# Performance work log

Measured on AMD Instinct MI355X. Metric: run time of the kernel, lower is better.

## Reference

```python
import jax, jax.numpy as jnp
import numpy as np

# WAGE-style quantizer (NeuroSim training path): round to 2^(b-1) levels, clip to (-1+1/S, 1-1/S),
# straight-through estimator for gradients.

def wage_q(x, bits=8):
    S = 2.0 ** (bits - 1)
    q = jnp.clip(jnp.round(x * S) / S, -1.0 + 1.0 / S, 1.0 - 1.0 / S)
    return x + jax.lax.stop_gradient(q - x)


def qconv(x, w, stride, pad, wl_w=8, wl_a=8):
    wq = wage_q(w, wl_w)
    y = jax.lax.conv_general_dilated(
        x, wq, window_strides=(stride, stride),
        padding=[(pad, pad), (pad, pad)],
        dimension_numbers=('NCHW', 'OIHW', 'NCHW'))
    return wage_q(y, wl_a)


def pad_hw(x, p):
    return jnp.pad(x, ((0, 0), (0, 0), (p, p), (p, p)))


def crop_like(x, tgt):
    return x[:, :, :tgt.shape[2], :tgt.shape[3]]


WEIGHT_SHAPES = {
    'w1': (64, 4, 3, 3), 'w2': (128, 64, 3, 3), 'w3': (256, 128, 3, 3), 'w4': (512, 256, 3, 3),
    'wr11': (512, 512, 3, 3), 'wr12': (512, 512, 3, 3), 'wr21': (512, 512, 3, 3), 'wr22': (512, 512, 3, 3),
    'wd3': (128, 512, 4, 4), 'wd2': (64, 416, 4, 4), 'wd1': (4, 224, 4, 4),
    'wu43': (32, 512, 4, 4), 'wu32': (32, 416, 4, 4), 'wu21': (32, 224, 4, 4), 'wu10': (32, 100, 4, 4),
    'wfc': (1, 32),
}


def setup_inputs() -> dict:
    key = jax.random.key(0)
    keys = jax.random.split(key, len(WEIGHT_SHAPES) + 1)
    inp = {'x': jax.random.normal(keys[0], (8, 4, 256, 256), dtype=jnp.float32)}
    for i, (name, shp) in enumerate(WEIGHT_SHAPES.items()):
        fan_in = int(np.prod(shp[1:]))
        inp[name] = jax.random.normal(keys[i + 1], shp, dtype=jnp.float32) / np.sqrt(fan_in)
    return inp


def reference(x, w1, w2, w3, w4, wr11, wr12, wr21, wr22,
              wd3, wd2, wd1, wu43, wu32, wu21, wu10, wfc):
    c1 = qconv(x, w1, 2, 1)        # [B,64,128,128]
    c2 = qconv(c1, w2, 2, 1)       # [B,128,64,64]
    c3 = qconv(c2, w3, 2, 1)       # [B,256,32,32]
    c4 = qconv(c3, w4, 2, 1)       # [B,512,16,16]
    r11 = qconv(c4, wr11, 1, 1)
    r12 = (1.0 - qconv(r11, wr12, 1, 1)) * c4
    r21 = qconv(r12, wr21, 1, 1)
    r22 = (1.0 - qconv(r21, wr22, 1, 1)) * r12
    r22p = pad_hw(r22, 8)                                   # [B,512,32,32]
    flow4_up = crop_like(qconv(r22p, wu43, 1, 2), c3)       # [B,32,32,32]
    d3 = crop_like(qconv(r22p, wd3, 1, 2), c3)              # [B,128,32,32]
    cat3 = pad_hw(jnp.concatenate([c3, d3, flow4_up], 1), 16)  # [B,416,64,64]
    flow3_up = crop_like(qconv(cat3, wu32, 1, 2), c2)
    d2 = crop_like(qconv(cat3, wd2, 1, 2), c2)
    cat2 = pad_hw(jnp.concatenate([c2, d2, flow3_up], 1), 32)  # [B,224,128,128]
    flow2_up = crop_like(qconv(cat2, wu21, 1, 2), c1)
    d1 = crop_like(qconv(cat2, wd1, 1, 2), c1)
    cat1 = pad_hw(jnp.concatenate([c1, d1, flow2_up], 1), 64)  # [B,100,256,256]
    u10 = qconv(cat1, wu10, 1, 2)                              # [B,32,257,257]
    feat = jnp.max(u10, axis=(2, 3))                           # AdaptiveMaxPool2d((1,1))
    out = wage_q(feat @ wage_q(wfc, 8).T, 8)                   # QLinear 32->1
    return out
```

## Files before the change

kernel.cpp:

```cpp
#include <hip/hip_runtime.h>

#define DEV __device__ __forceinline__

typedef __attribute__((ext_vector_type(4))) int i32x4;

DEV int wqi(float y) {
    int q = (int)rintf(y * 128.0f);
    return q < -127 ? -127 : (q > 127 ? 127 : q);
}
DEV unsigned encf(float f) { unsigned u = __float_as_uint(f); return (u & 0x80000000u) ? ~u : (u | 0x80000000u); }
DEV float decf(unsigned u) { return (u & 0x80000000u) ? __uint_as_float(u ^ 0x80000000u) : __uint_as_float(~u); }
DEV float wq8f(float x) {
    float q = rintf(x * 128.0f) * 0.0078125f;
    return fminf(fmaxf(q, -0.9921875f), 0.9921875f);
}

#define GLOAD16(g, l) __builtin_amdgcn_global_load_lds( \
    (const __attribute__((address_space(1))) void*)(g), \
    (__attribute__((address_space(3))) void*)(l), 16, 0, 0)

struct PackDesc {
    const float* w0; const float* w1; uint4* dst;
    int OC0, OC1, CinW, K, noct, nch64u, ndup;
};
struct PackArgs { PackDesc d[11]; int bofs[12]; };

__global__ void __launch_bounds__(256) k_packall(PackArgs a) {
    __shared__ unsigned char sb[16 * (64 * 16 + 4)];
    const int b = blockIdx.x;
    int i = 0;
    #pragma unroll
    for (int j = 1; j < 11; ++j) if (b >= a.bofs[j]) i = j;
    const PackDesc D = a.d[i];
    const int b2 = b - a.bofs[i];
    const int oct = b2 % D.noct;
    const int ch64u = b2 / D.noct;
    const int K2 = D.K * D.K;
    const int row_elems = 64 * K2;
    const int SSTR = row_elems + 4;
    const int QR = row_elems / 4;
    const int NQ = 16 * QR;
    const int cin0 = ch64u * 64;
    const int tid = threadIdx.x;

    for (int q = tid; q < NQ; q += 256) {
        const int r = q / QR, j = q - r * QR;
        const int oc = oct * 16 + r;
        const float* src = nullptr; int oci = 0;
        if (oc < D.OC0) { src = D.w0; oci = oc; }
        else if (oc < D.OC0 + D.OC1) { src = D.w1; oci = oc - D.OC0; }
        const int e0 = j * 4;
        float v[4] = {0.f, 0.f, 0.f, 0.f};
        if (src != nullptr) {
            const float* p = src + ((size_t)oci * D.CinW + cin0) * K2 + e0;
            const int cin_last = cin0 + (e0 + 3) / K2;
            if (cin_last < D.CinW) {
                const float4 f4 = *(const float4*)p;
                v[0] = f4.x; v[1] = f4.y; v[2] = f4.z; v[3] = f4.w;
            } else {
                #pragma unroll
                for (int e = 0; e < 4; ++e) {
                    const int cin = cin0 + (e0 + e) / K2;
                    if (cin < D.CinW) v[e] = p[e];
                }
            }
        }
        unsigned pk = 0;
        #pragma unroll
        for (int e = 0; e < 4; ++e) pk |= ((unsigned)(wqi(v[e]) & 255)) << (e * 8);
        *(unsigned*)&sb[r * SSTR + e0] = pk;
    }
    __syncthreads();

    const int outN = K2 * 64;
    for (int idx = tid; idx < outN; idx += 256) {
        const int kpos = idx >> 6, lane = idx & 63;
        const int l15 = lane & 15, g = lane >> 4;
        unsigned wd[4] = {0u, 0u, 0u, 0u};
        #pragma unroll
        for (int e = 0; e < 16; ++e) {
            const unsigned bval = sb[l15 * SSTR + (g * 16 + e) * K2 + kpos];
            wd[e >> 2] |= bval << ((e & 3) * 8);
        }
        uint4 u; u.x = wd[0]; u.y = wd[1]; u.z = wd[2]; u.w = wd[3];
        for (int d = 0; d < D.ndup; ++d) {
            const int ch64 = ch64u + d * D.nch64u;
            D.dst[((size_t)(ch64 * K2 + kpos) * D.noct + oct) * 64 + lane] = u;
        }
    }
}

__global__ void __launch_bounds__(256) k_conv1(const float* __restrict__ x, const float* __restrict__ w1,
                                               signed char* __restrict__ cat1) {
    __shared__ float sw2[36][64];
    __shared__ float sin_[4][17][17];
    const int tid = threadIdx.x;
    const int n = blockIdx.y;
    const int oh0 = (blockIdx.x >> 4) * 8, ow0 = (blockIdx.x & 15) * 8;
    for (int i = tid; i < 2304; i += 256) sw2[i % 36][i / 36] = wq8f(w1[i]);
    const int ih0 = oh0 * 2 - 1, iw0 = ow0 * 2 - 1;
    for (int i = tid; i < 4 * 289; i += 256) {
        const int c = i / 289, rem = i % 289, r = rem / 17, cc = rem % 17;
        const int ih = ih0 + r, iw = iw0 + cc;
        float v = 0.f;
        if ((unsigned)ih < 256u && (unsigned)iw < 256u) v = x[((size_t)(n * 4 + c) * 256 + ih) * 256 + iw];
        sin_[c][r][cc] = v;
    }
    __syncthreads();
    const int sp = tid & 63, ocg = tid >> 6;
    const int oh = sp >> 3, ow = sp & 7;
    float acc[16];
    #pragma unroll
    for (int j = 0; j < 16; ++j) acc[j] = 0.f;
    #pragma unroll
    for (int c = 0; c < 4; ++c)
    #pragma unroll
    for (int kh = 0; kh < 3; ++kh)
    #pragma unroll
    for (int kw = 0; kw < 3; ++kw) {
        const float v = sin_[c][oh * 2 + kh][ow * 2 + kw];
        const float4* wp4 = (const float4*)&sw2[c * 9 + kh * 3 + kw][ocg * 16];
        #pragma unroll
        for (int q = 0; q < 4; ++q) {
            const float4 wv = wp4[q];
            acc[q * 4 + 0] = fmaf(v, wv.x, acc[q * 4 + 0]);
            acc[q * 4 + 1] = fmaf(v, wv.y, acc[q * 4 + 1]);
            acc[q * 4 + 2] = fmaf(v, wv.z, acc[q * 4 + 2]);
            acc[q * 4 + 3] = fmaf(v, wv.w, acc[q * 4 + 3]);
        }
    }
    const size_t pix = ((size_t)(n * 128) + oh0 + oh) * 128 + ow0 + ow;
    unsigned wd[4] = {0u, 0u, 0u, 0u};
    #pragma unroll
    for (int j = 0; j < 16; ++j)
        wd[j >> 2] |= ((unsigned)(wqi(acc[j]) & 255)) << ((j & 3) * 8);
    uint4 u; u.x = wd[0]; u.y = wd[1]; u.z = wd[2]; u.w = wd[3];
    *(uint4*)(cat1 + pix * 112 + ocg * 16) = u;
}

__global__ void k_init(unsigned* __restrict__ feat, uint4* __restrict__ zbuf) {
    feat[threadIdx.x] = encf(-2.0f);
    if (threadIdx.x < 64) { uint4 z; z.x = z.y = z.z = z.w = 0u; zbuf[threadIdx.x] = z; }
}

__global__ void k_fc(const unsigned* __restrict__ feat, const float* __restrict__ wfc,
                     float* __restrict__ out) {
    int n = threadIdx.x;
    if (n < 8) {
        float s = 0.f;
        for (int c = 0; c < 32; ++c) s += decf(feat[n * 32 + c]) * wq8f(wfc[c]);
        out[n] = wq8f(s);
    }
}

template<int CMODE>
__global__ void __launch_bounds__(256) k_comb(const int* __restrict__ ps, int D, int G,
                                              int NP, int OC, double inv,
                                              signed char* __restrict__ dst, int dstr, int dch,
                                              const void* __restrict__ res, int rstr,
                                              signed char* __restrict__ dhl, int dhlstr,
                                              short* __restrict__ dj) {
    const int t = blockIdx.x * 256 + threadIdx.x;
    const int opc = OC / 4;
    const int total = NP * opc;
    if (t >= total) return;
    const int pix = t / opc, oc0 = (t - pix * opc) * 4;
    const size_t base = (size_t)pix * OC + oc0;
    const size_t NPOC = (size_t)NP * OC;
    long v[4] = {0, 0, 0, 0};
    int sidx = 0;
    for (int d = 0; d < D; ++d) {
        long s0 = 0, s1 = 0, s2 = 0, s3 = 0;
        for (int g = 0; g < G; ++g, ++sidx) {
            const int4 p = *(const int4*)(ps + sidx * NPOC + base);
            s0 += p.x; s1 += p.y; s2 += p.z; s3 += p.w;
        }
        v[0] = v[0] * 256 + s0; v[1] = v[1] * 256 + s1;
        v[2] = v[2] * 256 + s2; v[3] = v[3] * 256 + s3;
    }
    if constexpr (CMODE == 0) {
        unsigned pk = 0;
        #pragma unroll
        for (int j = 0; j < 4; ++j)
            pk |= (unsigned)(wqi((float)((double)v[j] * inv)) & 255) << (j * 8);
        *(unsigned*)(dst + (size_t)pix * dstr + dch + oc0) = pk;
    } else {
        #pragma unroll
        for (int j = 0; j < 4; ++j) {
            const int qi = wqi((float)((double)v[j] * inv));
            const int oc = oc0 + j;
            if constexpr (CMODE == 1) {
                const int rv = (int)((const signed char*)res)[(size_t)pix * rstr + oc];
                const int jj = (128 - qi) * rv;
                const int d0 = ((jj + 128) & 255) - 128;
                const int t1 = (jj - d0) >> 8;
                dhl[(size_t)pix * dhlstr + oc] = (signed char)t1;
                dhl[(size_t)pix * dhlstr + 512 + oc] = (signed char)d0;
                dj[(size_t)pix * 512 + oc] = (short)jj;
            } else {
                const int rv = (int)((const short*)res)[(size_t)pix * rstr + oc];
                const int jj = (128 - qi) * rv;
                const int d0 = ((jj + 128) & 255) - 128;
                const int t1 = (jj - d0) >> 8;
                const int d1 = ((t1 + 128) & 255) - 128;
                const int d2 = (t1 - d1) >> 8;
                dhl[(size_t)pix * dhlstr + oc] = (signed char)d2;
                dhl[(size_t)pix * dhlstr + 512 + oc] = (signed char)d1;
                dhl[(size_t)pix * dhlstr + 1024 + oc] = (signed char)d0;
            }
        }
    }
}

template<int K, int STR, int WM, int WN, int BN, int NBUF, int MODE>
__global__ void __launch_bounds__(256) k_mconv(
    const signed char* __restrict__ s0, int Ctot, int st0,
    int S, int padeff,
    const uint4* __restrict__ wqp, int noct,
    signed char* __restrict__ dst, int dstr, int dch,
    unsigned* __restrict__ feat, int* __restrict__ ps,
    const signed char* __restrict__ zbuf,
    int OCv, int OH, int OW, int TILES_W, int nch,
    int NT, int NOCG, int swzq, int ORD)
{
    constexpr int TH = WM * 4;
    constexpr int RH = (TH - 1) * STR + K, RW = 7 * STR + K;
    constexpr int UPPS = 5;
    constexpr int K2 = K * K;
    constexpr int NUS = RH * RW * UPPS;
    constexpr int ROUNDS = (NUS + 255) / 256;
    constexpr int NUPS = ROUNDS * 256;
    constexpr int AHEAD = NBUF - 1;
    __shared__ uint4 lds[NBUF * NUPS];
    __shared__ float sred[4][2][16];

    const int tid = threadIdx.x, lane = tid & 63, w = tid >> 6;
    const int wm = w % WM, wn = w / WM;
    const int l15 = lane & 15, g = lane >> 4;

    const int b = blockIdx.x;
    const int work = (b & 7) * swzq + (b >> 3);
    int tile, n, ocg, slice;
    if (ORD == 0) {
        ocg = work % NOCG; const int t2 = work / NOCG;
        tile = t2 % NT; const int t3 = t2 / NT;
        n = t3 & 7; slice = t3 >> 3;
    } else {
        tile = work % NT; const int t2 = work / NT;
        n = t2 & 7; const int t3 = t2 >> 3;
        ocg = t3 % NOCG; slice = t3 / NOCG;
    }
    const int cin_off = slice * nch * 64;
    const uint4* wqpS = wqp + (size_t)slice * nch * K2 * noct * 64;

    const int tileh = tile / TILES_W, tilew = tile % TILES_W;
    const int oh0 = tileh * TH, ow0 = tilew * 8;
    const int ih0 = oh0 * STR - padeff, iw0 = ow0 * STR - padeff;
    const int blk_oct0 = ocg * (WN * BN);

    int pixb[2];
    #pragma unroll
    for (int am = 0; am < 2; ++am) {
        const int sp = wm * 32 + am * 16 + l15;
        pixb[am] = ((sp >> 3) * STR) * RW + (sp & 7) * STR;
    }

    i32x4 acc[2][BN];
    #pragma unroll
    for (int am = 0; am < 2; ++am)
        #pragma unroll
        for (int bn = 0; bn < BN; ++bn) acc[am][bn] = (i32x4){0, 0, 0, 0};

    auto issue = [&](int ch, int buf) {
        uint4* lb = &lds[buf * NUPS];
        #pragma unroll
        for (int rd = 0; rd < ROUNDS; ++rd) {
            const int d = rd * 256 + tid;
            const signed char* gp = zbuf;
            if (d < NUS) {
                const int pix = d / UPPS;
                const int u = d - pix * UPPS;
                const int r = pix / RW, c = pix - r * RW;
                const int ih = ih0 + r, iw = iw0 + c;
                const int cin = cin_off + ch * 64 + u * 16;
                if (u < 4 && (unsigned)ih < (unsigned)S && (unsigned)iw < (unsigned)S && cin < Ctot)
                    gp = s0 + (((size_t)n * S + ih) * S + iw) * st0 + cin;
            }
            GLOAD16(gp, lb + rd * 256 + (tid & ~63));
        }
    };

    #pragma unroll
    for (int i = 0; i < AHEAD; ++i) if (i < nch) issue(i, i % NBUF);

    for (int ch = 0; ch < nch; ++ch) {
        if (ch + AHEAD < nch) issue(ch + AHEAD, (ch + AHEAD) % NBUF);
        const int infl = (nch - 1 - ch < AHEAD) ? nch - 1 - ch : AHEAD;
        if (infl >= 2)      __builtin_amdgcn_s_waitcnt(0xF70 | (2 * ROUNDS));
        else if (infl == 1) __builtin_amdgcn_s_waitcnt(0xF70 | ROUNDS);
        else                __builtin_amdgcn_s_waitcnt(0xF70);
        __builtin_amdgcn_s_barrier();
        __builtin_amdgcn_sched_barrier(0);
        const int bufo = (ch % NBUF) * NUPS;
        const int pb0 = bufo + pixb[0] * UPPS + g;
        const int pb1 = bufo + pixb[1] * UPPS + g;
        const size_t wbase = ((size_t)ch * K2 * noct + blk_oct0 + wn * BN) * 64 + lane;
        #pragma unroll
        for (int kpos = 0; kpos < K2; ++kpos) {
            const int kh = kpos / K, kw = kpos % K;
            const int po = (kh * RW + kw) * UPPS;
            i32x4 bfr[BN];
            #pragma unroll
            for (int bn = 0; bn < BN; ++bn) {
                union { uint4 u; i32x4 v; } bu;
                bu.u = wqpS[wbase + ((size_t)kpos * noct + bn) * 64];
                bfr[bn] = bu.v;
            }
            union { uint4 u; i32x4 v; } a0, a1;
            a0.u = lds[pb0 + po];
            a1.u = lds[pb1 + po];
            #pragma unroll
            for (int bn = 0; bn < BN; ++bn) {
                acc[0][bn] = __builtin_amdgcn_mfma_i32_16x16x64_i8(a0.v, bfr[bn], acc[0][bn], 0, 0, 0);
                acc[1][bn] = __builtin_amdgcn_mfma_i32_16x16x64_i8(a1.v, bfr[bn], acc[1][bn], 0, 0, 0);
            }
        }
        __builtin_amdgcn_sched_barrier(0);
        __builtin_amdgcn_s_barrier();
    }

    if constexpr (MODE == 2) {
        #pragma unroll
        for (int bn = 0; bn < BN; ++bn) {
            float m = -2.0f;
            #pragma unroll
            for (int am = 0; am < 2; ++am)
                #pragma unroll
                for (int rg = 0; rg < 4; ++rg) {
                    const int sp = wm * 32 + am * 16 + g * 4 + rg;
                    const int oh = oh0 + (sp >> 3), ow = ow0 + (sp & 7);
                    float v = -2.0f;
                    if (oh < OH && ow < OW) {
                        const float y = (float)acc[am][bn][rg] * (1.f / 16384.f);
                        v = (float)wqi(y) * 0.0078125f;
                    }
                    m = fmaxf(m, v);
                }
            m = fmaxf(m, __shfl_xor(m, 16));
            m = fmaxf(m, __shfl_xor(m, 32));
            if (lane < 16) sred[w][bn][l15] = m;
        }
        __syncthreads();
        if (tid < BN * 16) {
            const int bn = tid >> 4, l = tid & 15;
            float mm = sred[0][bn][l];
            #pragma unroll
            for (int i = 1; i < WM * WN; ++i) mm = fmaxf(mm, sred[i][bn][l]);
            atomicMax(&feat[n * 32 + (blk_oct0 + bn) * 16 + l], encf(mm));
        }
    } else if constexpr (MODE == 3) {
        #pragma unroll
        for (int am = 0; am < 2; ++am)
        #pragma unroll
        for (int bn = 0; bn < BN; ++bn)
        #pragma unroll
        for (int rg = 0; rg < 4; ++rg) {
            const int sp = wm * 32 + am * 16 + g * 4 + rg;
            const int oh = oh0 + (sp >> 3), ow = ow0 + (sp & 7);
            const int oc = (blk_oct0 + wn * BN + bn) * 16 + l15;
            if (oh < OH && ow < OW && oc < OCv) {
                ps[(((size_t)slice * 8 + n) * OH * OW + (size_t)oh * OW + ow) * OCv + oc] = acc[am][bn][rg];
            }
        }
    } else {
        #pragma unroll
        for (int am = 0; am < 2; ++am)
        #pragma unroll
        for (int bn = 0; bn < BN; ++bn)
        #pragma unroll
        for (int rg = 0; rg < 4; ++rg) {
            const int sp = wm * 32 + am * 16 + g * 4 + rg;
            const int oh = oh0 + (sp >> 3), ow = ow0 + (sp & 7);
            const int oc = (blk_oct0 + wn * BN + bn) * 16 + l15;
            if (oh < OH && ow < OW && oc < OCv) {
                const size_t pixo = (size_t)(n * OH + oh) * OW + ow;
                const float y = (float)acc[am][bn][rg] * (1.f / 16384.f);
                dst[pixo * dstr + dch + oc] = (signed char)wqi(y);
            }
        }
    }
}

extern "C" void kernel_launch(void* const* d_in, const int* in_sizes, int n_in,
                              void* d_out, int out_size, void* d_ws, size_t ws_size,
                              hipStream_t stream)
{
    (void)in_sizes; (void)n_in; (void)out_size; (void)ws_size;
    const float* x = (const float*)d_in[0];
    const float* wfc = (const float*)d_in[16];
    float* out = (float*)d_out;

    char* ws = (char*)d_ws;
    size_t off = 0;
    auto alloc = [&](size_t bytes) { char* p = ws + off; off += (bytes + 255) & ~(size_t)255; return p; };

    struct PH { int i0, OC0, i1, OC1, CinW, K, noct, nch64u, ndup; };
    static const PH ph[11] = {
        {2, 128, -1, 0,  64, 3,  8, 1, 1},
        {3, 256, -1, 0, 128, 3, 16, 2, 1},
        {4, 512, -1, 0, 256, 3, 32, 4, 1},
        {5, 512, -1, 0, 512, 3, 32, 8, 1},
        {6, 512, -1, 0, 512, 3, 32, 8, 1},
        {7, 512, -1, 0, 512, 3, 32, 8, 2},
        {8, 512, -1, 0, 512, 3, 32, 8, 1},
        {9, 128, 12, 32, 512, 4, 10, 8, 3},
        {10, 64, 13, 32, 416, 4,  6, 7, 1},
        {11,  4, 14, 32, 224, 4,  3, 4, 1},
        {15, 32, -1, 0, 100, 4,  2, 2, 1}};

    PackArgs pa;
    int bacc = 0;
    uint4* wp[11];
    for (int i = 0; i < 11; ++i) {
        const int nch64 = ph[i].nch64u * ph[i].ndup;
        const int nel = nch64 * ph[i].K * ph[i].K * ph[i].noct * 64;
        wp[i] = (uint4*)alloc((size_t)nel * 16);
        pa.d[i].w0 = (const float*)d_in[ph[i].i0];
        pa.d[i].w1 = (ph[i].i1 >= 0) ? (const float*)d_in[ph[i].i1] : nullptr;
        pa.d[i].dst = wp[i];
        pa.d[i].OC0 = ph[i].OC0; pa.d[i].OC1 = ph[i].OC1;
        pa.d[i].CinW = ph[i].CinW; pa.d[i].K = ph[i].K; pa.d[i].noct = ph[i].noct;
        pa.d[i].nch64u = ph[i].nch64u; pa.d[i].ndup = ph[i].ndup;
        pa.bofs[i] = bacc;
        bacc += ph[i].noct * ph[i].nch64u;
    }
    pa.bofs[11] = bacc;

    signed char* cat1b = (signed char*)alloc((size_t)8*128*128*112);
    signed char* cat2b = (signed char*)alloc((size_t)8*64*64*224);
    signed char* cat3b = (signed char*)alloc((size_t)8*32*32*416);
    signed char* c4b   = (signed char*)alloc((size_t)8*16*16*512);
    signed char* r11b  = (signed char*)alloc((size_t)8*16*16*512);
    signed char* r12d  = (signed char*)alloc((size_t)8*16*16*1024);
    short*       r12j  = (short*)alloc((size_t)8*16*16*512 * 2);
    signed char* r22d  = (signed char*)alloc((size_t)8*16*16*1536);
    int*         psum  = (int*)alloc((size_t)4*8*16*16*512 * 4);
    unsigned*    featb = (unsigned*)alloc(256 * 4);
    uint4*       zbuf  = (uint4*)alloc(1024);

    k_packall<<<dim3((unsigned)bacc), dim3(256), 0, stream>>>(pa);
    k_init<<<dim3(1), dim3(256), 0, stream>>>(featb, zbuf);
    k_conv1<<<dim3(256, 8), dim3(256), 0, stream>>>(x, (const float*)d_in[1], cat1b);

    const signed char* zb = (const signed char*)zbuf;
    const void* nv = nullptr;

    k_mconv<3,2,2,2,2,1,0><<<dim3(1024), 256, 0, stream>>>(
        cat1b,64,112, 128,1, wp[0],8, cat2b,224,0, nullptr,nullptr, zb,
        128,64,64,8, 1, 64,2,128, 0);
    k_mconv<3,2,2,2,2,2,0><<<dim3(512), 256, 0, stream>>>(
        cat2b,128,224, 64,1, wp[1],16, cat3b,416,0, nullptr,nullptr, zb,
        256,32,32,4, 2, 16,4,64, 0);
    k_mconv<3,2,2,2,2,1,3><<<dim3(1024), 256, 0, stream>>>(
        cat3b,256,416, 32,1, wp[2],32, nullptr,0,0, nullptr,(int*)psum, zb,
        512,16,16,2, 1, 4,8,128, 1);
    k_comb<0><<<dim3(1024), 256, 0, stream>>>(psum,1,4, 2048,512, 1.0/16384.0, c4b,512,0, nv,0, nullptr,0,nullptr);
    k_mconv<3,1,4,1,2,2,3><<<dim3(1024), 256, 0, stream>>>(
        c4b,512,512, 16,1, wp[3],32, nullptr,0,0, nullptr,psum, zb,
        512,16,16,2, 2, 2,16,128, 1);
    k_comb<0><<<dim3(1024), 256, 0, stream>>>(psum,1,4, 2048,512, 1.0/16384.0, r11b,512,0, nv,0, nullptr,0,nullptr);
    k_mconv<3,1,4,1,2,3,3><<<dim3(512), 256, 0, stream>>>(
        r11b,512,512, 16,1, wp[4],32, nullptr,0,0, nullptr,psum, zb,
        512,16,16,2, 4, 2,16,64, 1);
    k_comb<1><<<dim3(1024), 256, 0, stream>>>(psum,1,2, 2048,512, 1.0/16384.0, nullptr,0,0, c4b,512, r12d,1024,r12j);
    k_mconv<3,1,4,1,2,2,3><<<dim3(1024), 256, 0, stream>>>(
        r12d,1024,1024, 16,1, wp[5],32, nullptr,0,0, nullptr,psum, zb,
        512,16,16,2, 4, 2,16,128, 1);
    k_comb<0><<<dim3(1024), 256, 0, stream>>>(psum,2,2, 2048,512, 1.0/2097152.0, r11b,512,0, nv,0, nullptr,0,nullptr);
    k_mconv<3,1,4,1,2,3,3><<<dim3(512), 256, 0, stream>>>(
        r11b,512,512, 16,1, wp[6],32, nullptr,0,0, nullptr,psum, zb,
        512,16,16,2, 4, 2,16,64, 1);
    k_comb<2><<<dim3(1024), 256, 0, stream>>>(psum,1,2, 2048,512, 1.0/16384.0, nullptr,0,0, r12j,512, r22d,1536,nullptr);
    k_mconv<4,1,4,1,2,2,3><<<dim3(960), 256, 0, stream>>>(
        r22d,1536,1536, 16,10, wp[7],10, nullptr,0,0, nullptr,psum, zb,
        160,32,32,4, 8, 8,5,120, 1);
    k_comb<0><<<dim3(1280), 256, 0, stream>>>(psum,3,1, 8192,160, 1.0/268435456.0, cat3b,416,256, nv,0, nullptr,0,nullptr);
    k_mconv<4,1,4,1,2,2,0><<<dim3(768), 256, 0, stream>>>(
        cat3b,416,416, 32,18, wp[8],6, cat2b,224,128, nullptr,nullptr, zb,
        96,64,64,8, 7, 32,3,96, 0);
    k_mconv<4,1,4,1,3,2,0><<<dim3(1024), 256, 0, stream>>>(
        cat2b,224,224, 64,34, wp[9],3, cat1b,112,64, nullptr,nullptr, zb,
        48,128,128,16, 4, 128,1,128, 0);
    k_mconv<4,1,4,1,2,2,2><<<dim3(4488), 256, 0, stream>>>(
        cat1b,112,112, 128,66, wp[10],2, nullptr,0,0, featb,nullptr, zb,
        32,257,257,33, 2, 561,1,561, 0);
    k_fc<<<dim3(1), dim3(64), 0, stream>>>(featb, wfc, out);
}
```

Measured before the change: 344.8 us.

## Regroup packed weights per warp group and precompute load addresses

The weight packing kernel now stores each warp's output-channel group contiguously across all input-channel chunks and kernel positions, so each warp's B-fragment reads walk one contiguous stream instead of striding by the total octet count. The input-tile issue loop precomputes per-round base pointers and channel limits once per block, which removes per-chunk division and bounds arithmetic. The final max-pool epilogue reduces raw integer accumulators and quantizes only the block maximum, which is valid because quantization is monotonic. The cost is a more complex indexing contract between the packer and the conv kernels, with a new per-layer group size.

```diff
diff --git a/kernel.cpp b/kernel.cpp
--- a/kernel.cpp
+++ b/kernel.cpp
@@ -21,7 +21,7 @@
 
 struct PackDesc {
     const float* w0; const float* w1; uint4* dst;
-    int OC0, OC1, CinW, K, noct, nch64u, ndup;
+    int OC0, OC1, CinW, K, noct, nch64u, ndup, gsz;
 };
 struct PackArgs { PackDesc d[11]; int bofs[12]; };
 
@@ -36,12 +36,14 @@
     const int oct = b2 % D.noct;
     const int ch64u = b2 / D.noct;
     const int K2 = D.K * D.K;
+    const int NCHT = D.nch64u * D.ndup;
     const int row_elems = 64 * K2;
     const int SSTR = row_elems + 4;
     const int QR = row_elems / 4;
     const int NQ = 16 * QR;
     const int cin0 = ch64u * 64;
     const int tid = threadIdx.x;
+    const int og = oct / D.gsz, ol = oct % D.gsz;
 
     for (int q = tid; q < NQ; q += 256) {
         const int r = q / QR, j = q - r * QR;
@@ -85,7 +87,7 @@
         uint4 u; u.x = wd[0]; u.y = wd[1]; u.z = wd[2]; u.w = wd[3];
         for (int d = 0; d < D.ndup; ++d) {
             const int ch64 = ch64u + d * D.nch64u;
-            D.dst[((size_t)(ch64 * K2 + kpos) * D.noct + oct) * 64 + lane] = u;
+            D.dst[((size_t)((og * NCHT + ch64) * K2 + kpos) * D.gsz + ol) * 64 + lane] = u;
         }
     }
 }
@@ -216,7 +218,7 @@
 __global__ void __launch_bounds__(256) k_mconv(
     const signed char* __restrict__ s0, int Ctot, int st0,
     int S, int padeff,
-    const uint4* __restrict__ wqp, int noct,
+    const uint4* __restrict__ wqp, int nchtot,
     signed char* __restrict__ dst, int dstr, int dch,
     unsigned* __restrict__ feat, int* __restrict__ ps,
     const signed char* __restrict__ zbuf,
@@ -232,7 +234,7 @@
     constexpr int NUPS = ROUNDS * 256;
     constexpr int AHEAD = NBUF - 1;
     __shared__ uint4 lds[NBUF * NUPS];
-    __shared__ float sred[4][2][16];
+    __shared__ int sred[4][2][16];
 
     const int tid = threadIdx.x, lane = tid & 63, w = tid >> 6;
     const int wm = w % WM, wn = w / WM;
@@ -251,7 +253,7 @@
         ocg = t3 % NOCG; slice = t3 / NOCG;
     }
     const int cin_off = slice * nch * 64;
-    const uint4* wqpS = wqp + (size_t)slice * nch * K2 * noct * 64;
+    const int group = ocg * WN + wn;
 
     const int tileh = tile / TILES_W, tilew = tile % TILES_W;
     const int oh0 = tileh * TH, ow0 = tilew * 8;
@@ -265,6 +267,26 @@
         pixb[am] = ((sp >> 3) * STR) * RW + (sp & 7) * STR;
     }
 
+    int climit[ROUNDS];
+    const signed char* gpb[ROUNDS];
+    #pragma unroll
+    for (int rd = 0; rd < ROUNDS; ++rd) {
+        const int d = rd * 256 + tid;
+        int cl = -1;
+        const signed char* gb = zbuf;
+        if (d < NUS) {
+            const int pix = d / UPPS;
+            const int u = d - pix * UPPS;
+            const int r = pix / RW, c = pix - r * RW;
+            const int ih = ih0 + r, iw = iw0 + c;
+            if (u < 4 && (unsigned)ih < (unsigned)S && (unsigned)iw < (unsigned)S) {
+                cl = Ctot - cin_off - u * 16;
+                gb = s0 + (((size_t)n * S + ih) * S + iw) * st0 + cin_off + u * 16;
+            }
+        }
+        climit[rd] = cl; gpb[rd] = gb;
+    }
+
     i32x4 acc[2][BN];
     #pragma unroll
     for (int am = 0; am < 2; ++am)
@@ -273,19 +295,10 @@
 
     auto issue = [&](int ch, int buf) {
         uint4* lb = &lds[buf * NUPS];
+        const int ch64v = ch * 64;
         #pragma unroll
         for (int rd = 0; rd < ROUNDS; ++rd) {
-            const int d = rd * 256 + tid;
-            const signed char* gp = zbuf;
-            if (d < NUS) {
-                const int pix = d / UPPS;
-                const int u = d - pix * UPPS;
-                const int r = pix / RW, c = pix - r * RW;
-                const int ih = ih0 + r, iw = iw0 + c;
-                const int cin = cin_off + ch * 64 + u * 16;
-                if (u < 4 && (unsigned)ih < (unsigned)S && (unsigned)iw < (unsigned)S && cin < Ctot)
-                    gp = s0 + (((size_t)n * S + ih) * S + iw) * st0 + cin;
-            }
+            const signed char* gp = (ch64v < climit[rd]) ? (gpb[rd] + ch64v) : zbuf;
             GLOAD16(gp, lb + rd * 256 + (tid & ~63));
         }
     };
@@ -304,7 +317,7 @@
         const int bufo = (ch % NBUF) * NUPS;
         const int pb0 = bufo + pixb[0] * UPPS + g;
         const int pb1 = bufo + pixb[1] * UPPS + g;
-        const size_t wbase = ((size_t)ch * K2 * noct + blk_oct0 + wn * BN) * 64 + lane;
+        const uint4* wrow = wqp + ((size_t)(group * nchtot + slice * nch + ch) * K2 * BN) * 64 + lane;
         #pragma unroll
         for (int kpos = 0; kpos < K2; ++kpos) {
             const int kh = kpos / K, kw = kpos % K;
@@ -313,7 +326,7 @@
             #pragma unroll
             for (int bn = 0; bn < BN; ++bn) {
                 union { uint4 u; i32x4 v; } bu;
-                bu.u = wqpS[wbase + ((size_t)kpos * noct + bn) * 64];
+                bu.u = wrow[(kpos * BN + bn) * 64];
                 bfr[bn] = bu.v;
             }
             union { uint4 u; i32x4 v; } a0, a1;
@@ -332,31 +345,29 @@
     if constexpr (MODE == 2) {
         #pragma unroll
         for (int bn = 0; bn < BN; ++bn) {
-            float m = -2.0f;
+            int m = (int)0x80000000;
             #pragma unroll
             for (int am = 0; am < 2; ++am)
                 #pragma unroll
                 for (int rg = 0; rg < 4; ++rg) {
                     const int sp = wm * 32 + am * 16 + g * 4 + rg;
                     const int oh = oh0 + (sp >> 3), ow = ow0 + (sp & 7);
-                    float v = -2.0f;
-                    if (oh < OH && ow < OW) {
-                        const float y = (float)acc[am][bn][rg] * (1.f / 16384.f);
-                        v = (float)wqi(y) * 0.0078125f;
-                    }
-                    m = fmaxf(m, v);
+                    const int v = acc[am][bn][rg];
+                    if (oh < OH && ow < OW && v > m) m = v;
                 }
-            m = fmaxf(m, __shfl_xor(m, 16));
-            m = fmaxf(m, __shfl_xor(m, 32));
+            int o = __shfl_xor(m, 16); if (o > m) m = o;
+            o = __shfl_xor(m, 32); if (o > m) m = o;
             if (lane < 16) sred[w][bn][l15] = m;
         }
         __syncthreads();
         if (tid < BN * 16) {
             const int bn = tid >> 4, l = tid & 15;
-            float mm = sred[0][bn][l];
+            int mm = sred[0][bn][l];
             #pragma unroll
-            for (int i = 1; i < WM * WN; ++i) mm = fmaxf(mm, sred[i][bn][l]);
-            atomicMax(&feat[n * 32 + (blk_oct0 + bn) * 16 + l], encf(mm));
+            for (int i = 1; i < WM * WN; ++i) { const int o = sred[i][bn][l]; if (o > mm) mm = o; }
+            const float y = (float)mm * (1.f / 16384.f);
+            const float v = (float)wqi(y) * 0.0078125f;
+            atomicMax(&feat[n * 32 + (blk_oct0 + bn) * 16 + l], encf(v));
         }
     } else if constexpr (MODE == 3) {
         #pragma unroll
@@ -404,19 +415,19 @@
     size_t off = 0;
     auto alloc = [&](size_t bytes) { char* p = ws + off; off += (bytes + 255) & ~(size_t)255; return p; };
 
-    struct PH { int i0, OC0, i1, OC1, CinW, K, noct, nch64u, ndup; };
+    struct PH { int i0, OC0, i1, OC1, CinW, K, noct, nch64u, ndup, gsz; };
     static const PH ph[11] = {
-        {2, 128, -1, 0,  64, 3,  8, 1, 1},
-        {3, 256, -1, 0, 128, 3, 16, 2, 1},
-        {4, 512, -1, 0, 256, 3, 32, 4, 1},
-        {5, 512, -1, 0, 512, 3, 32, 8, 1},
-        {6, 512, -1, 0, 512, 3, 32, 8, 1},
-        {7, 512, -1, 0, 512, 3, 32, 8, 2},
-        {8, 512, -1, 0, 512, 3, 32, 8, 1},
-        {9, 128, 12, 32, 512, 4, 10, 8, 3},
-        {10, 64, 13, 32, 416, 4,  6, 7, 1},
-        {11,  4, 14, 32, 224, 4,  3, 4, 1},
-        {15, 32, -1, 0, 100, 4,  2, 2, 1}};
+        {2, 128, -1, 0,  64, 3,  8, 1, 1, 2},
+        {3, 256, -1, 0, 128, 3, 16, 2, 1, 2},
+        {4, 512, -1, 0, 256, 3, 32, 4, 1, 2},
+        {5, 512, -1, 0, 512, 3, 32, 8, 1, 2},
+        {6, 512, -1, 0, 512, 3, 32, 8, 1, 2},
+        {7, 512, -1, 0, 512, 3, 32, 8, 2, 2},
+        {8, 512, -1, 0, 512, 3, 32, 8, 1, 2},
+        {9, 128, 12, 32, 512, 4, 10, 8, 3, 2},
+        {10, 64, 13, 32, 416, 4,  6, 7, 1, 2},
+        {11,  4, 14, 32, 224, 4,  3, 4, 1, 3},
+        {15, 32, -1, 0, 100, 4,  2, 2, 1, 2}};
 
     PackArgs pa;
     int bacc = 0;
@@ -431,6 +442,7 @@
         pa.d[i].OC0 = ph[i].OC0; pa.d[i].OC1 = ph[i].OC1;
         pa.d[i].CinW = ph[i].CinW; pa.d[i].K = ph[i].K; pa.d[i].noct = ph[i].noct;
         pa.d[i].nch64u = ph[i].nch64u; pa.d[i].ndup = ph[i].ndup;
+        pa.d[i].gsz = ph[i].gsz;
         pa.bofs[i] = bacc;
         bacc += ph[i].noct * ph[i].nch64u;
     }
@@ -456,40 +468,40 @@
     const void* nv = nullptr;
 
     k_mconv<3,2,2,2,2,1,0><<<dim3(1024), 256, 0, stream>>>(
-        cat1b,64,112, 128,1, wp[0],8, cat2b,224,0, nullptr,nullptr, zb,
+        cat1b,64,112, 128,1, wp[0],1, cat2b,224,0, nullptr,nullptr, zb,
         128,64,64,8, 1, 64,2,128, 0);
     k_mconv<3,2,2,2,2,2,0><<<dim3(512), 256, 0, stream>>>(
-        cat2b,128,224, 64,1, wp[1],16, cat3b,416,0, nullptr,nullptr, zb,
+        cat2b,128,224, 64,1, wp[1],2, cat3b,416,0, nullptr,nullptr, zb,
         256,32,32,4, 2, 16,4,64, 0);
     k_mconv<3,2,2,2,2,1,3><<<dim3(1024), 256, 0, stream>>>(
-        cat3b,256,416, 32,1, wp[2],32, nullptr,0,0, nullptr,(int*)psum, zb,
+        cat3b,256,416, 32,1, wp[2],4, nullptr,0,0, nullptr,(int*)psum, zb,
         512,16,16,2, 1, 4,8,128, 1);
     k_comb<0><<<dim3(1024), 256, 0, stream>>>(psum,1,4, 2048,512, 1.0/16384.0, c4b,512,0, nv,0, nullptr,0,nullptr);
     k_mconv<3,1,4,1,2,2,3><<<dim3(1024), 256, 0, stream>>>(
-        c4b,512,512, 16,1, wp[3],32, nullptr,0,0, nullptr,psum, zb,
+        c4b,512,512, 16,1, wp[3],8, nullptr,0,0, nullptr,psum, zb,
         512,16,16,2, 2, 2,16,128, 1);
     k_comb<0><<<dim3(1024), 256, 0, stream>>>(psum,1,4, 2048,512, 1.0/16384.0, r11b,512,0, nv,0, nullptr,0,nullptr);
     k_mconv<3,1,4,1,2,3,3><<<dim3(512), 256, 0, stream>>>(
-        r11b,512,512, 16,1, wp[4],32, nullptr,0,0, nullptr,psum, zb,
+        r11b,512,512, 16,1, wp[4],8, nullptr,0,0, nullptr,psum, zb,
         512,16,16,2, 4, 2,16,64, 1);
     k_comb<1><<<dim3(1024), 256, 0, stream>>>(psum,1,2, 2048,512, 1.0/16384.0, nullptr,0,0, c4b,512, r12d,1024,r12j);
     k_mconv<3,1,4,1,2,2,3><<<dim3(1024), 256, 0, stream>>>(
-        r12d,1024,1024, 16,1, wp[5],32, nullptr,0,0, nullptr,psum, zb,
+        r12d,1024,1024, 16,1, wp[5],16, nullptr,0,0, nullptr,psum, zb,
         512,16,16,2, 4, 2,16,128, 1);
     k_comb<0><<<dim3(1024), 256, 0, stream>>>(psum,2,2, 2048,512, 1.0/2097152.0, r11b,512,0, nv,0, nullptr,0,nullptr);
     k_mconv<3,1,4,1,2,3,3><<<dim3(512), 256, 0, stream>>>(
-        r11b,512,512, 16,1, wp[6],32, nullptr,0,0, nullptr,psum, zb,
+        r11b,512,512, 16,1, wp[6],8, nullptr,0,0, nullptr,psum, zb,
         512,16,16,2, 4, 2,16,64, 1);
     k_comb<2><<<dim3(1024), 256, 0, stream>>>(psum,1,2, 2048,512, 1.0/16384.0, nullptr,0,0, r12j,512, r22d,1536,nullptr);
     k_mconv<4,1,4,1,2,2,3><<<dim3(960), 256, 0, stream>>>(
-        r22d,1536,1536, 16,10, wp[7],10, nullptr,0,0, nullptr,psum, zb,
+        r22d,1536,1536, 16,10, wp[7],24, nullptr,0,0, nullptr,psum, zb,
         160,32,32,4, 8, 8,5,120, 1);
     k_comb<0><<<dim3(1280), 256, 0, stream>>>(psum,3,1, 8192,160, 1.0/268435456.0, cat3b,416,256, nv,0, nullptr,0,nullptr);
     k_mconv<4,1,4,1,2,2,0><<<dim3(768), 256, 0, stream>>>(
-        cat3b,416,416, 32,18, wp[8],6, cat2b,224,128, nullptr,nullptr, zb,
+        cat3b,416,416, 32,18, wp[8],7, cat2b,224,128, nullptr,nullptr, zb,
         96,64,64,8, 7, 32,3,96, 0);
     k_mconv<4,1,4,1,3,2,0><<<dim3(1024), 256, 0, stream>>>(
-        cat2b,224,224, 64,34, wp[9],3, cat1b,112,64, nullptr,nullptr, zb,
+        cat2b,224,224, 64,34, wp[9],4, cat1b,112,64, nullptr,nullptr, zb,
         48,128,128,16, 4, 128,1,128, 0);
     k_mconv<4,1,4,1,2,2,2><<<dim3(4488), 256, 0, stream>>>(
         cat1b,112,112, 128,66, wp[10],2, nullptr,0,0, featb,nullptr, zb,
```

Result: faster. 333.4 us (-3.3%).
